# Kernel optimization log

Hardware: AMD Instinct MI355X
Metric: run time of the kernel (lower is better)

## Reference

```python
import jax, jax.numpy as jnp
import numpy as np


def gru_last(x, lens, Wg, bg, Wc, bc):
    """TF GRUCell scan over time, masked by lens; returns final hidden state.
    x: [N, T, D], lens: [N] int, Wg: [D+H, 2H], Wc: [D+H, H]. Returns [N, H]."""
    N, T, _ = x.shape
    H = bc.shape[0]
    xT = jnp.swapaxes(x, 0, 1)  # [T, N, D]

    def step(h, inp):
        xt, t = inp
        ru = jax.nn.sigmoid(jnp.concatenate([xt, h], axis=-1) @ Wg + bg)
        r, u = jnp.split(ru, 2, axis=-1)
        c = jnp.tanh(jnp.concatenate([xt, r * h], axis=-1) @ Wc + bc)
        hn = u * h + (1.0 - u) * c
        hn = jnp.where((t < lens)[:, None], hn, h)
        return hn, None

    h0 = jnp.zeros((N, H), x.dtype)
    hT, _ = jax.lax.scan(step, h0, (xT, jnp.arange(T)))
    return hT


def reverse_by_len(x, lens):
    """tf.reverse_sequence: reverse first lens[i] steps of each row. x: [N,T,D]."""
    T = x.shape[1]
    i = jnp.arange(T)[None, :]
    idx = jnp.where(i < lens[:, None], lens[:, None] - 1 - i, i)
    return jnp.take_along_axis(x, idx[:, :, None], axis=1)


def setup_inputs() -> dict:
    key = jax.random.key(0)
    ks = jax.random.split(key, 16)
    B, S, W = 64, 32, 64
    V, D, H, O = 50000, 128, 256, 5
    s = 0.05
    inp = {
        'X': jax.random.randint(ks[0], (B, S, W), 0, V, dtype=jnp.int32),
        'L': jnp.maximum(1, jax.random.randint(ks[1], (B, S), 0, W, dtype=jnp.int32)),
        'L2': jnp.maximum(1, jax.random.randint(ks[2], (B,), 0, S, dtype=jnp.int32)),
        'emb': jax.random.normal(ks[3], (V, D), jnp.float32) * s,
        'sWg_f': jax.random.normal(ks[4], (2 * D, 2 * D), jnp.float32) * s,
        'sbg_f': jnp.ones((2 * D,), jnp.float32),
        'sWc_f': jax.random.normal(ks[5], (2 * D, D), jnp.float32) * s,
        'sbc_f': jnp.zeros((D,), jnp.float32),
        'sWg_b': jax.random.normal(ks[6], (2 * D, 2 * D), jnp.float32) * s,
        'sbg_b': jnp.ones((2 * D,), jnp.float32),
        'sWc_b': jax.random.normal(ks[7], (2 * D, D), jnp.float32) * s,
        'sbc_b': jnp.zeros((D,), jnp.float32),
        'dWg_f': jax.random.normal(ks[8], (2 * D + H, 2 * H), jnp.float32) * s,
        'dbg_f': jnp.ones((2 * H,), jnp.float32),
        'dWc_f': jax.random.normal(ks[9], (2 * D + H, H), jnp.float32) * s,
        'dbc_f': jnp.zeros((H,), jnp.float32),
        'dWg_b': jax.random.normal(ks[10], (2 * D + H, 2 * H), jnp.float32) * s,
        'dbg_b': jnp.ones((2 * H,), jnp.float32),
        'dWc_b': jax.random.normal(ks[11], (2 * D + H, H), jnp.float32) * s,
        'dbc_b': jnp.zeros((H,), jnp.float32),
        'W1': jax.random.normal(ks[12], (2 * H, H), jnp.float32) * s,
        'b1': jnp.zeros((H,), jnp.float32),
        'W2': jax.random.normal(ks[13], (H, O), jnp.float32) * s,
        'b2': jnp.zeros((O,), jnp.float32),
    }
    return inp


def reference(X, L, L2, emb,
              sWg_f, sbg_f, sWc_f, sbc_f, sWg_b, sbg_b, sWc_b, sbc_b,
              dWg_f, dbg_f, dWc_f, dbc_f, dWg_b, dbg_b, dWc_b, dbc_b,
              W1, b1, W2, b2):
    B, S, W = X.shape
    D = emb.shape[1]
    # word embeddings: [B, S, W, D] -> flatten sentences to rows
    words = emb[X].reshape(B * S, W, D)
    ls = L.reshape(B * S)
    # sentence-level bi-GRU, gather final valid states
    fw = gru_last(words, ls, sWg_f, sbg_f, sWc_f, sbc_f)
    bw = gru_last(reverse_by_len(words, ls), ls, sWg_b, sbg_b, sWc_b, sbc_b)
    sent = jnp.concatenate([fw, bw], axis=-1).reshape(B, S, 2 * D)
    # document-level bi-GRU over sentence vectors
    fw_d = gru_last(sent, L2, dWg_f, dbg_f, dWc_f, dbc_f)
    bw_d = gru_last(reverse_by_len(sent, L2), L2, dWg_b, dbg_b, dWc_b, dbc_b)
    doc = jnp.concatenate([fw_d, bw_d], axis=-1)  # [B, 2H]
    # MLP head
    hidden = jax.nn.relu(doc @ W1 + b1)
    logits = hidden @ W2 + b2
    return logits
```

## Files before the change

### kernel.cpp

```cpp
#include <hip/hip_runtime.h>
#include <cstdint>
#include <cstddef>


typedef __attribute__((ext_vector_type(8))) short bf16x8;
typedef __attribute__((ext_vector_type(8))) _Float16 f16x8;
typedef __attribute__((ext_vector_type(4))) float f32x4;

__device__ __forceinline__ void split_bf16(float f, short& hi, short& lo) {
  unsigned u = __float_as_uint(f);
  unsigned rb = (u + 0x7FFFu + ((u >> 16) & 1u)) & 0xFFFF0000u;
  hi = (short)(rb >> 16);
  float r = f - __uint_as_float(rb);
  unsigned ur = __float_as_uint(r);
  lo = (short)((ur + 0x7FFFu + ((ur >> 16) & 1u)) >> 16);
}

__device__ __forceinline__ float sigm(float x) { return 1.f / (1.f + __expf(-x)); }
__device__ __forceinline__ float tanh_fast(float x) {
  float e = __expf(2.f * x);
  return 1.f - 2.f / (e + 1.f);
}

__global__ void bt_prep(const float* __restrict__ sWg_f, const float* __restrict__ sWc_f,
                        const float* __restrict__ sWg_b, const float* __restrict__ sWc_b,
                        short* __restrict__ BtHi, short* __restrict__ BtLo) {
  int i = blockIdx.x * 256 + threadIdx.x;
  if (i >= 768 * 128) return;
  int n = i >> 7, k = i & 127;
  float f;
  if (n < 256) f = sWg_f[k * 256 + n];
  else if (n < 384) f = sWc_f[k * 128 + (n - 256)];
  else if (n < 640) f = sWg_b[k * 256 + (n - 384)];
  else f = sWc_b[k * 128 + (n - 640)];
  short hi, lo;
  split_bf16(f, hi, lo);
  BtHi[i] = hi;
  BtLo[i] = lo;
}

__global__ void packdt_prep(const float* __restrict__ dWg_f, const float* __restrict__ dWc_f,
                            const float* __restrict__ dWg_b, const float* __restrict__ dWc_b,
                            short* __restrict__ Hi, short* __restrict__ Lo) {
  int i = blockIdx.x * 256 + threadIdx.x;
  if (i >= 1536 * 256) return;
  int n = i >> 8, k = i & 255;
  float f;
  if (n < 512) f = dWg_f[k * 512 + n];
  else if (n < 768) f = dWc_f[k * 256 + (n - 512)];
  else if (n < 1280) f = dWg_b[k * 512 + (n - 768)];
  else f = dWc_b[k * 256 + (n - 1280)];
  short hi, lo;
  split_bf16(f, hi, lo);
  Hi[i] = hi;
  Lo[i] = lo;
}

__global__ __launch_bounds__(256, 1) void emb_gemm(
    const float* __restrict__ emb, const short* __restrict__ BtHi,
    const short* __restrict__ BtLo, float* __restrict__ C) {
  const int tid = threadIdx.x;
  const int w = tid >> 6, l = tid & 63, li = l & 15, g = l >> 4;
  const int m0 = blockIdx.x * 64;

  bf16x8 ahi[4][4], alo[4][4];
#pragma unroll
  for (int mt = 0; mt < 4; ++mt) {
    int row = m0 + 16 * mt + li;
    if (row > 49999) row = 49999;
    const float* ap = emb + (size_t)row * 128 + 8 * g;
#pragma unroll
    for (int kk = 0; kk < 4; ++kk) {
      float4 v0 = *(const float4*)(ap + 32 * kk);
      float4 v1 = *(const float4*)(ap + 32 * kk + 4);
      float vv[8] = {v0.x, v0.y, v0.z, v0.w, v1.x, v1.y, v1.z, v1.w};
#pragma unroll
      for (int e = 0; e < 8; ++e) {
        short hi, lo;
        split_bf16(vv[e], hi, lo);
        ahi[mt][kk][e] = hi;
        alo[mt][kk][e] = lo;
      }
    }
  }

  f32x4 acc[4][12];
#pragma unroll
  for (int mt = 0; mt < 4; ++mt)
#pragma unroll
    for (int nt = 0; nt < 12; ++nt) acc[mt][nt] = (f32x4){0.f, 0.f, 0.f, 0.f};

#pragma unroll
  for (int nt = 0; nt < 12; ++nt) {
    const int col = 192 * w + 16 * nt + li;
    const short* bh = BtHi + col * 128 + 8 * g;
    const short* bl = BtLo + col * 128 + 8 * g;
    bf16x8 bhi[4], blo[4];
#pragma unroll
    for (int kk = 0; kk < 4; ++kk) {
      bhi[kk] = *(const bf16x8*)(bh + 32 * kk);
      blo[kk] = *(const bf16x8*)(bl + 32 * kk);
    }
#pragma unroll
    for (int kk = 0; kk < 4; ++kk)
#pragma unroll
      for (int mt = 0; mt < 4; ++mt) {
        acc[mt][nt] = __builtin_amdgcn_mfma_f32_16x16x32_bf16(alo[mt][kk], bhi[kk], acc[mt][nt], 0, 0, 0);
        acc[mt][nt] = __builtin_amdgcn_mfma_f32_16x16x32_bf16(ahi[mt][kk], blo[kk], acc[mt][nt], 0, 0, 0);
        acc[mt][nt] = __builtin_amdgcn_mfma_f32_16x16x32_bf16(ahi[mt][kk], bhi[kk], acc[mt][nt], 0, 0, 0);
      }
  }

#pragma unroll
  for (int mt = 0; mt < 4; ++mt)
#pragma unroll
    for (int nt = 0; nt < 12; ++nt) {
      const int col = 192 * w + 16 * nt + li;
#pragma unroll
      for (int r = 0; r < 4; ++r) {
        int row = m0 + 16 * mt + 4 * g + r;
        if (row < 50000) C[(size_t)row * 768 + col] = acc[mt][nt][r];
      }
    }
}

__global__ __launch_bounds__(256, 1) void xproj_gemm(
    const short* __restrict__ AHi, const short* __restrict__ ALo,
    const short* __restrict__ BtHi, const short* __restrict__ BtLo,
    float* __restrict__ C) {
  const int tid = threadIdx.x;
  const int w = tid >> 6, l = tid & 63, li = l & 15, g = l >> 4;
  const int m0 = blockIdx.x * 64;
  const int n0 = blockIdx.y * 512 + 128 * w;

  f32x4 acc[4][8];
#pragma unroll
  for (int mt = 0; mt < 4; ++mt)
#pragma unroll
    for (int nt = 0; nt < 8; ++nt) acc[mt][nt] = (f32x4){0.f, 0.f, 0.f, 0.f};

#pragma unroll
  for (int kk = 0; kk < 8; ++kk) {
    bf16x8 ah[4], al[4];
#pragma unroll
    for (int mt = 0; mt < 4; ++mt) {
      const int row = m0 + 16 * mt + li;
      ah[mt] = *(const bf16x8*)&AHi[(size_t)row * 256 + 32 * kk + 8 * g];
      al[mt] = *(const bf16x8*)&ALo[(size_t)row * 256 + 32 * kk + 8 * g];
    }
#pragma unroll
    for (int nt = 0; nt < 8; ++nt) {
      const int col = n0 + 16 * nt + li;
      bf16x8 bh = *(const bf16x8*)&BtHi[(size_t)col * 256 + 32 * kk + 8 * g];
      bf16x8 bl = *(const bf16x8*)&BtLo[(size_t)col * 256 + 32 * kk + 8 * g];
#pragma unroll
      for (int mt = 0; mt < 4; ++mt) {
        acc[mt][nt] = __builtin_amdgcn_mfma_f32_16x16x32_bf16(al[mt], bh, acc[mt][nt], 0, 0, 0);
        acc[mt][nt] = __builtin_amdgcn_mfma_f32_16x16x32_bf16(ah[mt], bl, acc[mt][nt], 0, 0, 0);
        acc[mt][nt] = __builtin_amdgcn_mfma_f32_16x16x32_bf16(ah[mt], bh, acc[mt][nt], 0, 0, 0);
      }
    }
  }

#pragma unroll
  for (int mt = 0; mt < 4; ++mt)
#pragma unroll
    for (int nt = 0; nt < 8; ++nt) {
      const int col = n0 + 16 * nt + li;
#pragma unroll
      for (int r = 0; r < 4; ++r) {
        int row = m0 + 16 * mt + 4 * g + r;
        C[(size_t)row * 1536 + col] = acc[mt][nt][r];
      }
    }
}

#define SENTS 16

__global__ __launch_bounds__(256, 1) void sent_gru(
    const int* __restrict__ X, const int* __restrict__ L,
    const float* __restrict__ embProj,
    const float* __restrict__ Wg_f, const float* __restrict__ bg_f,
    const float* __restrict__ Wc_f, const float* __restrict__ bc_f,
    const float* __restrict__ Wg_b, const float* __restrict__ bg_b,
    const float* __restrict__ Wc_b, const float* __restrict__ bc_b,
    short* __restrict__ sentHi, short* __restrict__ sentLo) {
  const int dir = blockIdx.y;
  const int g0 = blockIdx.x * SENTS;
  const int tid = threadIdx.x;
  const int w = tid >> 6, l = tid & 63;
  const int li = l & 15, g = l >> 4;
  const float* Wg = dir ? Wg_b : Wg_f;
  const float* Wc = dir ? Wc_b : Wc_f;
  const float* bgp = dir ? bg_b : bg_f;
  const float* bcp = dir ? bc_b : bc_f;

  __shared__ float xbuf[2][SENTS][384];
  __shared__ float h_f[SENTS][132];
  __shared__ float u_f[SENTS][132];
  alignas(16) __shared__ short h_hi[SENTS][136], h_lo[SENTS][136];
  alignas(16) __shared__ short rh_hi[SENTS][136], rh_lo[SENTS][136];
  __shared__ int wid[2][SENTS];
  __shared__ int len_s[SENTS];

  bf16x8 bgh[4][4], bgl[4][4];
  bf16x8 bch[2][4], bcl[2][4];
#pragma unroll
  for (int nt = 0; nt < 4; ++nt)
#pragma unroll
    for (int kk = 0; kk < 4; ++kk) {
      const float* base = Wg + (size_t)(128 + 32 * kk + 8 * g) * 256 + 64 * w + 16 * nt + li;
#pragma unroll
      for (int e = 0; e < 8; ++e) {
        short hi, lo;
        split_bf16(base[(size_t)e * 256], hi, lo);
        bgh[nt][kk][e] = hi; bgl[nt][kk][e] = lo;
      }
    }
#pragma unroll
  for (int ct = 0; ct < 2; ++ct)
#pragma unroll
    for (int kk = 0; kk < 4; ++kk) {
      const float* base = Wc + (size_t)(128 + 32 * kk + 8 * g) * 128 + 32 * w + 16 * ct + li;
#pragma unroll
      for (int e = 0; e < 8; ++e) {
        short hi, lo;
        split_bf16(base[(size_t)e * 128], hi, lo);
        bch[ct][kk][e] = hi; bcl[ct][kk][e] = lo;
      }
    }
  float bgj[4], bcj[2];
#pragma unroll
  for (int nt = 0; nt < 4; ++nt) bgj[nt] = bgp[64 * w + 16 * nt + li];
#pragma unroll
  for (int ct = 0; ct < 2; ++ct) bcj[ct] = bcp[32 * w + 16 * ct + li];

  if (tid < SENTS) {
    int ll = L[g0 + tid];
    len_s[tid] = ll;
    wid[0][tid] = X[(g0 + tid) * 64 + (dir ? (ll - 1) : 0)];
    wid[1][tid] = (1 < ll) ? X[(g0 + tid) * 64 + (dir ? (ll - 2) : 1)] : 0;
  }
  for (int q = tid; q < SENTS * 136; q += 256) {
    ((short*)h_hi)[q] = 0; ((short*)h_lo)[q] = 0;
  }
  for (int q = tid; q < SENTS * 132; q += 256) ((float*)h_f)[q] = 0.f;
  __syncthreads();

  int lens4[4];
#pragma unroll
  for (int r = 0; r < 4; ++r) lens4[r] = len_s[4 * g + r];
  int maxlen = 0;
#pragma unroll
  for (int m = 0; m < SENTS; ++m) maxlen = max(maxlen, len_s[m]);

  auto prefetch_x = [&](int t) {
    int b = t & 1;
#pragma unroll
    for (int c = 0; c < 6; ++c) {
      int q = tid + 256 * c;
      int m = q / 96, s = q - m * 96;
      const float* src = embProj + (size_t)wid[b][m] * 768 + dir * 384 + s * 4;
      float* dst = (float*)&xbuf[b][0][0] + q * 4;
      __builtin_amdgcn_global_load_lds(
          (const __attribute__((address_space(1))) void*)src,
          (__attribute__((address_space(3))) void*)dst, 16, 0, 0);
    }
  };

  prefetch_x(0);
  __syncthreads();

  for (int t = 0; t < maxlen; ++t) {
    const int cur = t & 1;
    prefetch_x(t + 1);
    if (tid < SENTS) {
      int ll = len_s[tid], tt = t + 2;
      wid[tt & 1][tid] = (tt < ll) ? X[(g0 + tid) * 64 + (dir ? (ll - 1 - tt) : tt)] : 0;
    }

    bf16x8 a_hi[4], a_lo[4];
#pragma unroll
    for (int kk = 0; kk < 4; ++kk) {
      a_hi[kk] = *(const bf16x8*)&h_hi[li][32 * kk + 8 * g];
      a_lo[kk] = *(const bf16x8*)&h_lo[li][32 * kk + 8 * g];
    }
    f32x4 accg[4];
#pragma unroll
    for (int nt = 0; nt < 4; ++nt) {
      const int col = 64 * w + 16 * nt + li;
      f32x4 c;
#pragma unroll
      for (int r = 0; r < 4; ++r) c[r] = bgj[nt] + xbuf[cur][4 * g + r][col];
#pragma unroll
      for (int kk = 0; kk < 4; ++kk) {
        c = __builtin_amdgcn_mfma_f32_16x16x32_bf16(a_hi[kk], bgh[nt][kk], c, 0, 0, 0);
        c = __builtin_amdgcn_mfma_f32_16x16x32_bf16(a_hi[kk], bgl[nt][kk], c, 0, 0, 0);
        c = __builtin_amdgcn_mfma_f32_16x16x32_bf16(a_lo[kk], bgh[nt][kk], c, 0, 0, 0);
      }
      accg[nt] = c;
    }
    if (w < 2) {
#pragma unroll
      for (int nt = 0; nt < 4; ++nt) {
        const int col = 64 * w + 16 * nt + li;
#pragma unroll
        for (int r = 0; r < 4; ++r) {
          const int row = 4 * g + r;
          float s = sigm(accg[nt][r]);
          float rh = s * h_f[row][col];
          short hi, lo;
          split_bf16(rh, hi, lo);
          rh_hi[row][col] = hi;
          rh_lo[row][col] = lo;
        }
      }
    } else {
#pragma unroll
      for (int nt = 0; nt < 4; ++nt) {
        const int col = 64 * (w - 2) + 16 * nt + li;
#pragma unroll
        for (int r = 0; r < 4; ++r) {
          u_f[4 * g + r][col] = sigm(accg[nt][r]);
        }
      }
    }
    __syncthreads();

    bf16x8 ra_hi[4], ra_lo[4];
#pragma unroll
    for (int kk = 0; kk < 4; ++kk) {
      ra_hi[kk] = *(const bf16x8*)&rh_hi[li][32 * kk + 8 * g];
      ra_lo[kk] = *(const bf16x8*)&rh_lo[li][32 * kk + 8 * g];
    }
#pragma unroll
    for (int ct = 0; ct < 2; ++ct) {
      const int col = 32 * w + 16 * ct + li;
      f32x4 c;
#pragma unroll
      for (int r = 0; r < 4; ++r) c[r] = bcj[ct] + xbuf[cur][4 * g + r][256 + col];
#pragma unroll
      for (int kk = 0; kk < 4; ++kk) {
        c = __builtin_amdgcn_mfma_f32_16x16x32_bf16(ra_hi[kk], bch[ct][kk], c, 0, 0, 0);
        c = __builtin_amdgcn_mfma_f32_16x16x32_bf16(ra_hi[kk], bcl[ct][kk], c, 0, 0, 0);
        c = __builtin_amdgcn_mfma_f32_16x16x32_bf16(ra_lo[kk], bch[ct][kk], c, 0, 0, 0);
      }
#pragma unroll
      for (int r = 0; r < 4; ++r) {
        const int row = 4 * g + r;
        float cand = tanh_fast(c[r]);
        float u = u_f[row][col];
        float hold = h_f[row][col];
        float hn = u * hold + (1.f - u) * cand;
        hn = (t < lens4[r]) ? hn : hold;
        h_f[row][col] = hn;
        short hi, lo;
        split_bf16(hn, hi, lo);
        h_hi[row][col] = hi;
        h_lo[row][col] = lo;
      }
    }
    __syncthreads();
  }

  for (int q = tid; q < SENTS * 128; q += 256) {
    int m = q >> 7, j = q & 127;
    size_t o = (size_t)(g0 + m) * 256 + dir * 128 + j;
    sentHi[o] = h_hi[m][j];
    sentLo[o] = h_lo[m][j];
  }
}

#define DOCS 16

__global__ __launch_bounds__(512, 1) void doc_gru_mfma(
    const float* __restrict__ xprojD, const int* __restrict__ L2,
    const float* __restrict__ dWg_f, const float* __restrict__ dbg_f,
    const float* __restrict__ dWc_f, const float* __restrict__ dbc_f,
    const float* __restrict__ dWg_b, const float* __restrict__ dbg_b,
    const float* __restrict__ dWc_b, const float* __restrict__ dbc_b,
    float* __restrict__ docv) {
  const int dir = blockIdx.y;
  const int g0 = blockIdx.x * DOCS;
  const int tid = threadIdx.x;
  const int w = tid >> 6, l = tid & 63, li = l & 15, g = l >> 4;
  const float* Wg = dir ? dWg_b : dWg_f;
  const float* Wc = dir ? dWc_b : dWc_f;
  const float* bgp = dir ? dbg_b : dbg_f;
  const float* bcp = dir ? dbc_b : dbc_f;
  const int xoff = dir ? 768 : 0;

  alignas(16) __shared__ short h_hi[DOCS][264];
  alignas(16) __shared__ short rh_hi[DOCS][264];
  __shared__ float h_f[DOCS][256], u_f[DOCS][256];
  __shared__ int len_s[DOCS];

  f16x8 wg[4][8];
  f16x8 wc[2][8];
  const float* Wg_h = Wg + 256 * 512;
  const float* Wc_h = Wc + 256 * 256;
#pragma unroll
  for (int nt = 0; nt < 4; ++nt)
#pragma unroll
    for (int kk = 0; kk < 8; ++kk) {
      const float* base = Wg_h + (size_t)(32 * kk + 8 * g) * 512 + 64 * w + 16 * nt + li;
#pragma unroll
      for (int e = 0; e < 8; ++e) wg[nt][kk][e] = (_Float16)base[(size_t)e * 512];
      asm volatile("" : "+v"(wg[nt][kk]));
    }
#pragma unroll
  for (int ct = 0; ct < 2; ++ct)
#pragma unroll
    for (int kk = 0; kk < 8; ++kk) {
      const float* base = Wc_h + (size_t)(32 * kk + 8 * g) * 256 + 32 * w + 16 * ct + li;
#pragma unroll
      for (int e = 0; e < 8; ++e) wc[ct][kk][e] = (_Float16)base[(size_t)e * 256];
      asm volatile("" : "+v"(wc[ct][kk]));
    }
  float bgj[4], bcj[2];
#pragma unroll
  for (int nt = 0; nt < 4; ++nt) bgj[nt] = bgp[64 * w + 16 * nt + li];
#pragma unroll
  for (int ct = 0; ct < 2; ++ct) bcj[ct] = bcp[32 * w + 16 * ct + li];

  if (tid < DOCS) len_s[tid] = L2[g0 + tid];
  for (int q = tid; q < DOCS * 264; q += 512) ((short*)h_hi)[q] = 0;
  for (int q = tid; q < DOCS * 256; q += 512) {
    ((float*)h_f)[q] = 0.f; ((float*)u_f)[q] = 0.f;
  }
  __syncthreads();

  int lens4[4];
#pragma unroll
  for (int r = 0; r < 4; ++r) lens4[r] = len_s[4 * g + r];
  int maxlen = 0;
#pragma unroll
  for (int m = 0; m < DOCS; ++m) maxlen = max(maxlen, len_s[m]);

  auto xrow = [&](int r, int t) -> size_t {
    int ti = dir ? max(lens4[r] - 1 - t, 0) : min(t, 31);
    return ((size_t)(g0 + 4 * g + r) * 32 + ti) * 1536 + xoff;
  };

  float xg[16], xc[8], xgn[16], xcn[8];
#pragma unroll
  for (int r = 0; r < 4; ++r) {
    size_t xb = xrow(r, 0);
#pragma unroll
    for (int nt = 0; nt < 4; ++nt) xg[nt * 4 + r] = xprojD[xb + 64 * w + 16 * nt + li];
#pragma unroll
    for (int ct = 0; ct < 2; ++ct) xc[ct * 4 + r] = xprojD[xb + 512 + 32 * w + 16 * ct + li];
  }

  for (int t = 0; t < maxlen; ++t) {
    f32x4 acc[4];
#pragma unroll
    for (int nt = 0; nt < 4; ++nt)
#pragma unroll
      for (int r = 0; r < 4; ++r) acc[nt][r] = bgj[nt] + xg[nt * 4 + r];
    f32x4 acc2[2];
#pragma unroll
    for (int ct = 0; ct < 2; ++ct)
#pragma unroll
      for (int r = 0; r < 4; ++r) acc2[ct][r] = bcj[ct] + xc[ct * 4 + r];

#pragma unroll
    for (int r = 0; r < 4; ++r) {
      size_t xb = xrow(r, t + 1);
#pragma unroll
      for (int nt = 0; nt < 4; ++nt) xgn[nt * 4 + r] = xprojD[xb + 64 * w + 16 * nt + li];
#pragma unroll
      for (int ct = 0; ct < 2; ++ct) xcn[ct * 4 + r] = xprojD[xb + 512 + 32 * w + 16 * ct + li];
    }

#pragma unroll
    for (int c = 0; c < 8; ++c) {
      f16x8 ah = *(const f16x8*)&h_hi[li][32 * c + 8 * g];
#pragma unroll
      for (int nt = 0; nt < 4; ++nt)
        acc[nt] = __builtin_amdgcn_mfma_f32_16x16x32_f16(ah, wg[nt][c], acc[nt], 0, 0, 0);
    }
    if (w < 4) {
#pragma unroll
      for (int nt = 0; nt < 4; ++nt) {
        const int col = 64 * w + 16 * nt + li;
#pragma unroll
        for (int r = 0; r < 4; ++r) {
          const int m = 4 * g + r;
          float s = sigm(acc[nt][r]);
          float rh = s * h_f[m][col];
          rh_hi[m][col] = __builtin_bit_cast(short, (_Float16)rh);
        }
      }
    } else {
#pragma unroll
      for (int nt = 0; nt < 4; ++nt) {
        const int col = 64 * (w - 4) + 16 * nt + li;
#pragma unroll
        for (int r = 0; r < 4; ++r) u_f[4 * g + r][col] = sigm(acc[nt][r]);
      }
    }
    __syncthreads();

#pragma unroll
    for (int c = 0; c < 8; ++c) {
      f16x8 rah = *(const f16x8*)&rh_hi[li][32 * c + 8 * g];
#pragma unroll
      for (int ct = 0; ct < 2; ++ct)
        acc2[ct] = __builtin_amdgcn_mfma_f32_16x16x32_f16(rah, wc[ct][c], acc2[ct], 0, 0, 0);
    }
#pragma unroll
    for (int ct = 0; ct < 2; ++ct) {
      const int col = 32 * w + 16 * ct + li;
#pragma unroll
      for (int r = 0; r < 4; ++r) {
        const int m = 4 * g + r;
        float cand = tanh_fast(acc2[ct][r]);
        float u = u_f[m][col];
        float hold = h_f[m][col];
        float hn = u * hold + (1.f - u) * cand;
        hn = (t < lens4[r]) ? hn : hold;
        h_f[m][col] = hn;
        h_hi[m][col] = __builtin_bit_cast(short, (_Float16)hn);
      }
    }
    __syncthreads();

#pragma unroll
    for (int i = 0; i < 16; ++i) xg[i] = xgn[i];
#pragma unroll
    for (int i = 0; i < 8; ++i) xc[i] = xcn[i];
  }

  for (int q = tid; q < DOCS * 256; q += 512) {
    int m = q >> 8, j = q & 255;
    docv[(size_t)(g0 + m) * 512 + dir * 256 + j] = h_f[m][j];
  }
}

__global__ __launch_bounds__(256) void mlp_head(
    const float* __restrict__ docv, const float* __restrict__ W1,
    const float* __restrict__ b1, const float* __restrict__ W2,
    const float* __restrict__ b2, float* __restrict__ out) {
  const int b = blockIdx.x, j = threadIdx.x;
  __shared__ float hid[256];
  float acc = b1[j];
#pragma unroll 4
  for (int k = 0; k < 512; ++k) acc += docv[b * 512 + k] * W1[k * 256 + j];
  hid[j] = fmaxf(acc, 0.f);
  __syncthreads();
  if (j < 5) {
    float a = b2[j];
#pragma unroll 4
    for (int k = 0; k < 256; ++k) a += hid[k] * W2[k * 5 + j];
    out[b * 5 + j] = a;
  }
}

extern "C" void kernel_launch(void* const* d_in, const int* in_sizes, int n_in,
                              void* d_out, int out_size, void* d_ws, size_t ws_size,
                              hipStream_t stream) {
  const int* X = (const int*)d_in[0];
  const int* L = (const int*)d_in[1];
  const int* L2 = (const int*)d_in[2];
  const float* emb = (const float*)d_in[3];
  const float* sWg_f = (const float*)d_in[4];
  const float* sbg_f = (const float*)d_in[5];
  const float* sWc_f = (const float*)d_in[6];
  const float* sbc_f = (const float*)d_in[7];
  const float* sWg_b = (const float*)d_in[8];
  const float* sbg_b = (const float*)d_in[9];
  const float* sWc_b = (const float*)d_in[10];
  const float* sbc_b = (const float*)d_in[11];
  const float* dWg_f = (const float*)d_in[12];
  const float* dbg_f = (const float*)d_in[13];
  const float* dWc_f = (const float*)d_in[14];
  const float* dbc_f = (const float*)d_in[15];
  const float* dWg_b = (const float*)d_in[16];
  const float* dbg_b = (const float*)d_in[17];
  const float* dWc_b = (const float*)d_in[18];
  const float* dbc_b = (const float*)d_in[19];
  const float* W1 = (const float*)d_in[20];
  const float* b1 = (const float*)d_in[21];
  const float* W2 = (const float*)d_in[22];
  const float* b2 = (const float*)d_in[23];
  float* out = (float*)d_out;

  float* ws = (float*)d_ws;
  float* embProj = ws;
  float* xprojD = embProj + 38400000;
  float* docv = xprojD + 3145728;
  short* sentHi = (short*)(docv + 32768);
  short* sentLo = sentHi + 524288;
  short* BtHi = sentLo + 524288;
  short* BtLo = BtHi + 98304;
  short* PdTHi = BtLo + 98304;
  short* PdTLo = PdTHi + 393216;

  hipLaunchKernelGGL(bt_prep, dim3(384), dim3(256), 0, stream,
                     sWg_f, sWc_f, sWg_b, sWc_b, BtHi, BtLo);
  hipLaunchKernelGGL(packdt_prep, dim3(1536), dim3(256), 0, stream,
                     dWg_f, dWc_f, dWg_b, dWc_b, PdTHi, PdTLo);

  hipLaunchKernelGGL(emb_gemm, dim3(782), dim3(256), 0, stream,
                     emb, BtHi, BtLo, embProj);

  hipLaunchKernelGGL(sent_gru, dim3(128, 2), dim3(256), 0, stream,
                     X, L, embProj,
                     sWg_f, sbg_f, sWc_f, sbc_f,
                     sWg_b, sbg_b, sWc_b, sbc_b, sentHi, sentLo);

  hipLaunchKernelGGL(xproj_gemm, dim3(32, 3), dim3(256), 0, stream,
                     sentHi, sentLo, PdTHi, PdTLo, xprojD);

  hipLaunchKernelGGL(doc_gru_mfma, dim3(4, 2), dim3(512), 0, stream,
                     xprojD, L2,
                     dWg_f, dbg_f, dWc_f, dbc_f,
                     dWg_b, dbg_b, dWc_b, dbc_b, docv);

  hipLaunchKernelGGL(mlp_head, dim3(64), dim3(256), 0, stream,
                     docv, W1, b1, W2, b2, out);
}
```

Baseline: 774.9 us.

## Pre-pack doc GRU weights, drop fp32 hidden copy, raise sent_gru occupancy

Adds a prep kernel that packs the doc-level recurrent weights into per-thread fp16 vector order, so doc_gru_mfma loads them with one vector load each instead of strided scalar gathers. In sent_gru the fp32 hidden-state array is dropped and the old hidden state is rebuilt from the bf16 hi/lo pair, which cuts LDS use and allows launch bounds of two blocks per CU. The cost is an extra launch and scratch buffer, a small precision change from the hi/lo reconstruction, and possible register spills under the tighter bound.

Result: slower. 1.146 ms (+47.9%).

```diff
diff --git a/kernel.cpp b/kernel.cpp
--- a/kernel.cpp
+++ b/kernel.cpp
@@ -14,6 +14,10 @@
   float r = f - __uint_as_float(rb);
   unsigned ur = __float_as_uint(r);
   lo = (short)((ur + 0x7FFFu + ((ur >> 16) & 1u)) >> 16);
+}
+
+__device__ __forceinline__ float bf2f(short s) {
+  return __uint_as_float(((unsigned)(unsigned short)s) << 16);
 }
 
 __device__ __forceinline__ float sigm(float x) { return 1.f / (1.f + __expf(-x)); }
@@ -56,6 +60,30 @@
   Lo[i] = lo;
 }
 
+__global__ void dw_prep(const float* __restrict__ dWg_f, const float* __restrict__ dWc_f,
+                        const float* __restrict__ dWg_b, const float* __restrict__ dWc_b,
+                        short* __restrict__ DW) {
+  int i = blockIdx.x * 256 + threadIdx.x;
+  if (i >= 393216) return;
+  int e = i & 7;
+  int tid = (i >> 3) & 511;
+  int f = (i >> 12) & 63;
+  int dir = i >> 12 >= 48 ? 1 : 0;
+  f = (i >> 12) - dir * 48;
+  int w = tid >> 6, g = (tid >> 4) & 3, li = tid & 15;
+  const float* Wg = dir ? dWg_b : dWg_f;
+  const float* Wc = dir ? dWc_b : dWc_f;
+  float v;
+  if (f < 32) {
+    int nt = f >> 3, kk = f & 7;
+    v = Wg[(size_t)(256 + 32 * kk + 8 * g + e) * 512 + 64 * w + 16 * nt + li];
+  } else {
+    int q = f - 32, ct = q >> 3, kk = q & 7;
+    v = Wc[(size_t)(256 + 32 * kk + 8 * g + e) * 256 + 32 * w + 16 * ct + li];
+  }
+  DW[i] = __builtin_bit_cast(short, (_Float16)v);
+}
+
 __global__ __launch_bounds__(256, 1) void emb_gemm(
     const float* __restrict__ emb, const short* __restrict__ BtHi,
     const short* __restrict__ BtLo, float* __restrict__ C) {
@@ -177,7 +205,7 @@
 
 #define SENTS 16
 
-__global__ __launch_bounds__(256, 1) void sent_gru(
+__global__ __launch_bounds__(256, 2) void sent_gru(
     const int* __restrict__ X, const int* __restrict__ L,
     const float* __restrict__ embProj,
     const float* __restrict__ Wg_f, const float* __restrict__ bg_f,
@@ -196,7 +224,6 @@
   const float* bcp = dir ? bc_b : bc_f;
 
   __shared__ float xbuf[2][SENTS][384];
-  __shared__ float h_f[SENTS][132];
   __shared__ float u_f[SENTS][132];
   alignas(16) __shared__ short h_hi[SENTS][136], h_lo[SENTS][136];
   alignas(16) __shared__ short rh_hi[SENTS][136], rh_lo[SENTS][136];
@@ -244,7 +271,6 @@
   for (int q = tid; q < SENTS * 136; q += 256) {
     ((short*)h_hi)[q] = 0; ((short*)h_lo)[q] = 0;
   }
-  for (int q = tid; q < SENTS * 132; q += 256) ((float*)h_f)[q] = 0.f;
   __syncthreads();
 
   int lens4[4];
@@ -308,7 +334,8 @@
         for (int r = 0; r < 4; ++r) {
           const int row = 4 * g + r;
           float s = sigm(accg[nt][r]);
-          float rh = s * h_f[row][col];
+          float hold = bf2f(h_hi[row][col]) + bf2f(h_lo[row][col]);
+          float rh = s * hold;
           short hi, lo;
           split_bf16(rh, hi, lo);
           rh_hi[row][col] = hi;
@@ -350,10 +377,9 @@
         const int row = 4 * g + r;
         float cand = tanh_fast(c[r]);
         float u = u_f[row][col];
-        float hold = h_f[row][col];
+        float hold = bf2f(h_hi[row][col]) + bf2f(h_lo[row][col]);
         float hn = u * hold + (1.f - u) * cand;
         hn = (t < lens4[r]) ? hn : hold;
-        h_f[row][col] = hn;
         short hi, lo;
         split_bf16(hn, hi, lo);
         h_hi[row][col] = hi;
@@ -375,17 +401,14 @@
 
 __global__ __launch_bounds__(512, 1) void doc_gru_mfma(
     const float* __restrict__ xprojD, const int* __restrict__ L2,
-    const float* __restrict__ dWg_f, const float* __restrict__ dbg_f,
-    const float* __restrict__ dWc_f, const float* __restrict__ dbc_f,
-    const float* __restrict__ dWg_b, const float* __restrict__ dbg_b,
-    const float* __restrict__ dWc_b, const float* __restrict__ dbc_b,
+    const short* __restrict__ DW,
+    const float* __restrict__ dbg_f, const float* __restrict__ dbc_f,
+    const float* __restrict__ dbg_b, const float* __restrict__ dbc_b,
     float* __restrict__ docv) {
   const int dir = blockIdx.y;
   const int g0 = blockIdx.x * DOCS;
   const int tid = threadIdx.x;
   const int w = tid >> 6, l = tid & 63, li = l & 15, g = l >> 4;
-  const float* Wg = dir ? dWg_b : dWg_f;
-  const float* Wc = dir ? dWc_b : dWc_f;
   const float* bgp = dir ? dbg_b : dbg_f;
   const float* bcp = dir ? dbc_b : dbc_f;
   const int xoff = dir ? 768 : 0;
@@ -397,24 +420,21 @@
 
   f16x8 wg[4][8];
   f16x8 wc[2][8];
-  const float* Wg_h = Wg + 256 * 512;
-  const float* Wc_h = Wc + 256 * 256;
+  const short* DWp = DW + (size_t)dir * 48 * 512 * 8;
 #pragma unroll
   for (int nt = 0; nt < 4; ++nt)
 #pragma unroll
     for (int kk = 0; kk < 8; ++kk) {
-      const float* base = Wg_h + (size_t)(32 * kk + 8 * g) * 512 + 64 * w + 16 * nt + li;
-#pragma unroll
-      for (int e = 0; e < 8; ++e) wg[nt][kk][e] = (_Float16)base[(size_t)e * 512];
+      int f = nt * 8 + kk;
+      wg[nt][kk] = *(const f16x8*)&DWp[((size_t)f * 512 + tid) * 8];
       asm volatile("" : "+v"(wg[nt][kk]));
     }
 #pragma unroll
   for (int ct = 0; ct < 2; ++ct)
 #pragma unroll
     for (int kk = 0; kk < 8; ++kk) {
-      const float* base = Wc_h + (size_t)(32 * kk + 8 * g) * 256 + 32 * w + 16 * ct + li;
-#pragma unroll
-      for (int e = 0; e < 8; ++e) wc[ct][kk][e] = (_Float16)base[(size_t)e * 256];
+      int f = 32 + ct * 8 + kk;
+      wc[ct][kk] = *(const f16x8*)&DWp[((size_t)f * 512 + tid) * 8];
       asm volatile("" : "+v"(wc[ct][kk]));
     }
   float bgj[4], bcj[2];
@@ -596,11 +616,14 @@
   short* BtLo = BtHi + 98304;
   short* PdTHi = BtLo + 98304;
   short* PdTLo = PdTHi + 393216;
+  short* DW = PdTLo + 393216;
 
   hipLaunchKernelGGL(bt_prep, dim3(384), dim3(256), 0, stream,
                      sWg_f, sWc_f, sWg_b, sWc_b, BtHi, BtLo);
   hipLaunchKernelGGL(packdt_prep, dim3(1536), dim3(256), 0, stream,
                      dWg_f, dWc_f, dWg_b, dWc_b, PdTHi, PdTLo);
+  hipLaunchKernelGGL(dw_prep, dim3(1536), dim3(256), 0, stream,
+                     dWg_f, dWc_f, dWg_b, dWc_b, DW);
 
   hipLaunchKernelGGL(emb_gemm, dim3(782), dim3(256), 0, stream,
                      emb, BtHi, BtLo, embProj);
@@ -614,9 +637,8 @@
                      sentHi, sentLo, PdTHi, PdTLo, xprojD);
 
   hipLaunchKernelGGL(doc_gru_mfma, dim3(4, 2), dim3(512), 0, stream,
-                     xprojD, L2,
-                     dWg_f, dbg_f, dWc_f, dbc_f,
-                     dWg_b, dbg_b, dWc_b, dbc_b, docv);
+                     xprojD, L2, DW,
+                     dbg_f, dbc_f, dbg_b, dbc_b, docv);
 
   hipLaunchKernelGGL(mlp_head, dim3(64), dim3(256), 0, stream,
                      docv, W1, b1, W2, b2, out);
```
